# Kernel tuning notes

Hardware: AMD Instinct MI355X
Metric: run time of the kernel (lower is better)

Reference implementation:

```python
import jax, jax.numpy as jnp
import numpy as np

D = 1024
H = 16
HD = D // H
FF = 4096
B = 4
S = 1024
EPS = 1e-5


def layer_norm(x, g, b):
    mu = jnp.mean(x, axis=-1, keepdims=True)
    var = jnp.mean(jnp.square(x - mu), axis=-1, keepdims=True)
    return (x - mu) * jax.lax.rsqrt(var + EPS) * g + b


def setup_inputs() -> dict:
    key = jax.random.key(0)
    ks = jax.random.split(key, 16)
    s = 0.02
    return {
        "src": jax.random.normal(ks[0], (B, S, D), jnp.float32),
        "attn_bias": jax.random.normal(ks[1], (H, S, S), jnp.float32),
        "Wqkv": jax.random.normal(ks[2], (3 * D, D), jnp.float32) * s,
        "bqkv": jnp.zeros((3 * D,), jnp.float32),
        "Wo": jax.random.normal(ks[3], (D, D), jnp.float32) * s,
        "bo": jnp.zeros((D,), jnp.float32),
        "g1": jnp.ones((D,), jnp.float32),
        "b1n": jnp.zeros((D,), jnp.float32),
        "g2": jnp.ones((D,), jnp.float32),
        "b2n": jnp.zeros((D,), jnp.float32),
        "W1": jax.random.normal(ks[4], (FF, D), jnp.float32) * s,
        "b1": jnp.zeros((FF,), jnp.float32),
        "W2": jax.random.normal(ks[5], (D, FF), jnp.float32) * s,
        "b2": jnp.zeros((D,), jnp.float32),
    }


def reference(src, attn_bias, Wqkv, bqkv, Wo, bo, g1, b1n, g2, b2n, W1, b1, W2, b2):
    bsz, seq, _ = src.shape
    qkv = src @ Wqkv.T + bqkv                      # [B,S,3D]
    q, k, v = jnp.split(qkv, 3, axis=-1)
    q = q.reshape(bsz, seq, H, HD)
    k = k.reshape(bsz, seq, H, HD)
    v = v.reshape(bsz, seq, H, HD)
    scores = jnp.einsum('bthd,bshd->bhts', q, k) / np.sqrt(HD).astype(np.float32)
    scores = scores + attn_bias[None]              # 3D bias broadcast over batch
    w = jax.nn.softmax(scores, axis=-1)
    ctx = jnp.einsum('bhts,bshd->bthd', w, v).reshape(bsz, seq, D)
    attn_out = ctx @ Wo.T + bo
    x = layer_norm(src + attn_out, g1, b1n)
    ff = (jax.nn.gelu(x @ W1.T + b1, approximate=False)) @ W2.T + b2
    return layer_norm(x + ff, g2, b2n)
```

## Files before the change

### kernel.cpp

```cpp
#include <hip/hip_runtime.h>
#include <cstdint>

typedef unsigned short u16;
typedef __bf16 bf16x8 __attribute__((ext_vector_type(8)));
typedef float f32x4 __attribute__((ext_vector_type(4)));
typedef unsigned short u16x8 __attribute__((ext_vector_type(8)));
typedef unsigned short u16x4 __attribute__((ext_vector_type(4)));

__device__ __forceinline__ u16 f2b(float f) {
  union { float f; unsigned u; } x; x.f = f;
  unsigned r = (x.u + 0x7FFFu + ((x.u >> 16) & 1u)) >> 16;
  return (u16)r;
}
__device__ __forceinline__ float b2f(u16 v) {
  union { unsigned u; float f; } x; x.u = (unsigned)v << 16; return x.f;
}

__device__ __forceinline__ void gload_lds16(const void* g, void* l) {
  __builtin_amdgcn_global_load_lds(
      (__attribute__((address_space(1))) void*)(uintptr_t)g,
      (__attribute__((address_space(3))) void*)(uintptr_t)l, 16, 0, 0);
}

struct CastArgs {
  const float* in[5];
  u16* out[5];
  int cum[6];
};
__global__ void cast_multi(CastArgs a) {
  const int i = blockIdx.x * 256 + threadIdx.x;
  int r = 0;
#pragma unroll
  for (int k = 1; k < 5; ++k) r += (i >= a.cum[k]);
  const int local = i - a.cum[r];
  const float4 v0 = *(const float4*)(a.in[r] + (size_t)local * 8);
  const float4 v1 = *(const float4*)(a.in[r] + (size_t)local * 8 + 4);
  u16x8 o = {f2b(v0.x), f2b(v0.y), f2b(v0.z), f2b(v0.w),
             f2b(v1.x), f2b(v1.y), f2b(v1.z), f2b(v1.w)};
  *(u16x8*)(a.out[r] + (size_t)local * 8) = o;
}

template<bool GELU_ACT, bool WRITE_VT>
__global__ void gemm_nt(const u16* __restrict__ A, const u16* __restrict__ Bw,
                        const float* __restrict__ bias, u16* __restrict__ Cb,
                        u16* __restrict__ Vt, int M, int N, int K) {
  __shared__ u16 As[2][128 * 32];
  __shared__ u16 Bs[2][128 * 32];
  const int tid = threadIdx.x;
  const int lane = tid & 63, wid = tid >> 6;
  const int bm = blockIdx.y * 128, bn = blockIdx.x * 128;
  const int wm = wid >> 1, wn = wid & 1;
  const int r = lane & 15, g = lane >> 4;
  const int s4 = (r >> 1) & 3;

  auto stage = [&](int buf, int k0) {
#pragma unroll
    for (int i = 0; i < 2; ++i) {
      const int c = tid + i * 256;
      const int row = c >> 2, ch = c & 3;
      const int gs = ch ^ ((row >> 1) & 3);
      gload_lds16(A + (size_t)(bm + row) * K + k0 + gs * 8, &As[buf][c * 8]);
      gload_lds16(Bw + (size_t)(bn + row) * K + k0 + gs * 8, &Bs[buf][c * 8]);
    }
  };

  f32x4 acc[4][4] = {};
  stage(0, 0);
  __syncthreads();
  const int nk = K >> 5;
  int cur = 0;
  for (int kt = 0; kt < nk; ++kt) {
    if (kt + 1 < nk) stage(cur ^ 1, (kt + 1) * 32);
    bf16x8 af[4], bfr[4];
#pragma unroll
    for (int m = 0; m < 4; ++m)
      af[m] = *(const bf16x8*)&As[cur][(wm * 64 + m * 16 + r) * 32 + (g ^ s4) * 8];
#pragma unroll
    for (int n = 0; n < 4; ++n)
      bfr[n] = *(const bf16x8*)&Bs[cur][(wn * 64 + n * 16 + r) * 32 + (g ^ s4) * 8];
#pragma unroll
    for (int m = 0; m < 4; ++m)
#pragma unroll
      for (int n = 0; n < 4; ++n)
        acc[m][n] = __builtin_amdgcn_mfma_f32_16x16x32_bf16(af[m], bfr[n], acc[m][n], 0, 0, 0);
    __syncthreads();
    cur ^= 1;
  }
#pragma unroll
  for (int m = 0; m < 4; ++m) {
    const int row0 = bm + wm * 64 + m * 16 + g * 4;
#pragma unroll
    for (int n = 0; n < 4; ++n) {
      const int col = bn + wn * 64 + n * 16 + r;
      const float bv = bias[col];
      if (WRITE_VT && col >= 2048) {
        const int hv = col - 2048;
        const int bb = row0 >> 10, s0 = row0 & 1023;
        u16x4 ov;
#pragma unroll
        for (int j = 0; j < 4; ++j) ov[j] = f2b(acc[m][n][j] + bv);
        *(u16x4*)(Vt + (((size_t)(bb * 16 + (hv >> 6))) * 64 + (hv & 63)) * 1024 + s0) = ov;
      } else {
#pragma unroll
        for (int j = 0; j < 4; ++j) {
          float v = acc[m][n][j] + bv;
          if (GELU_ACT) v = 0.5f * v * (1.f + erff(v * 0.70710678118654752f));
          Cb[(size_t)(row0 + j) * N + col] = f2b(v);
        }
      }
    }
  }
}

__global__ void gemm_nt_splitk(const u16* __restrict__ A, const u16* __restrict__ Bw,
                               u16* __restrict__ parts, int M, int N, int K, int Kc) {
  __shared__ u16 As[2][128 * 32];
  __shared__ u16 Bs[2][128 * 32];
  const int tid = threadIdx.x;
  const int lane = tid & 63, wid = tid >> 6;
  const int bm = blockIdx.y * 128, bn = blockIdx.x * 128;
  const int kbase = blockIdx.z * Kc;
  const int wm = wid >> 1, wn = wid & 1;
  const int r = lane & 15, g = lane >> 4;
  const int s4 = (r >> 1) & 3;

  auto stage = [&](int buf, int k0) {
#pragma unroll
    for (int i = 0; i < 2; ++i) {
      const int c = tid + i * 256;
      const int row = c >> 2, ch = c & 3;
      const int gs = ch ^ ((row >> 1) & 3);
      gload_lds16(A + (size_t)(bm + row) * K + k0 + gs * 8, &As[buf][c * 8]);
      gload_lds16(Bw + (size_t)(bn + row) * K + k0 + gs * 8, &Bs[buf][c * 8]);
    }
  };

  f32x4 acc[4][4] = {};
  stage(0, kbase);
  __syncthreads();
  const int nk = Kc >> 5;
  int cur = 0;
  for (int kt = 0; kt < nk; ++kt) {
    if (kt + 1 < nk) stage(cur ^ 1, kbase + (kt + 1) * 32);
    bf16x8 af[4], bfr[4];
#pragma unroll
    for (int m = 0; m < 4; ++m)
      af[m] = *(const bf16x8*)&As[cur][(wm * 64 + m * 16 + r) * 32 + (g ^ s4) * 8];
#pragma unroll
    for (int n = 0; n < 4; ++n)
      bfr[n] = *(const bf16x8*)&Bs[cur][(wn * 64 + n * 16 + r) * 32 + (g ^ s4) * 8];
#pragma unroll
    for (int m = 0; m < 4; ++m)
#pragma unroll
      for (int n = 0; n < 4; ++n)
        acc[m][n] = __builtin_amdgcn_mfma_f32_16x16x32_bf16(af[m], bfr[n], acc[m][n], 0, 0, 0);
    __syncthreads();
    cur ^= 1;
  }
  u16* Cp = parts + (size_t)blockIdx.z * M * N;
#pragma unroll
  for (int m = 0; m < 4; ++m) {
    const int row0 = bm + wm * 64 + m * 16 + g * 4;
#pragma unroll
    for (int n = 0; n < 4; ++n) {
      const int col = bn + wn * 64 + n * 16 + r;
#pragma unroll
      for (int j = 0; j < 4; ++j)
        Cp[(size_t)(row0 + j) * N + col] = f2b(acc[m][n][j]);
    }
  }
}

__global__ __launch_bounds__(256) void attn_kernel(
    const u16* __restrict__ qkv, const u16* __restrict__ Vt,
    const float* __restrict__ bias, u16* __restrict__ ctx) {
  const int fid = blockIdx.x;
  const int xcd = fid & 7, slot = fid >> 3;
  const int G = xcd * 64 + (slot >> 2);
  const int b = slot & 3;
  const int h = G >> 5;
  const int q0 = (G & 31) * 32;
  const int tid = threadIdx.x;
  const int lane = tid & 63, wid = tid >> 6;
  const int r = lane & 15, g = lane >> 4;
  const int bh = b * 16 + h;

  __shared__ __align__(16) u16 PB[2][16 * 1024];

  const size_t qb0 = (size_t)(b * 1024 + q0 + r) * 3072 + h * 64;
  const size_t qb1 = (size_t)(b * 1024 + q0 + 16 + r) * 3072 + h * 64;
  const bf16x8 aq00 = *(const bf16x8*)(qkv + qb0 + g * 8);
  const bf16x8 aq01 = *(const bf16x8*)(qkv + qb0 + 32 + g * 8);
  const bf16x8 aq10 = *(const bf16x8*)(qkv + qb1 + g * 8);
  const bf16x8 aq11 = *(const bf16x8*)(qkv + qb1 + 32 + g * 8);

  const int n0 = wid * 256;

  const u16* kptr = qkv + (size_t)(b * 1024 + n0 + r) * 3072 + 1024 + h * 64;
  const size_t kstep = (size_t)16 * 3072;
  bf16x8 k0a = *(const bf16x8*)(kptr + g * 8);
  bf16x8 k1a = *(const bf16x8*)(kptr + 32 + g * 8);
#pragma unroll
  for (int nt = 0; nt < 16; ++nt) {
    bf16x8 k0b, k1b;
    if (nt + 1 < 16) {
      const u16* kn = kptr + (size_t)(nt + 1) * kstep;
      k0b = *(const bf16x8*)(kn + g * 8);
      k1b = *(const bf16x8*)(kn + 32 + g * 8);
    }
    f32x4 a0 = {0.f, 0.f, 0.f, 0.f}, a1 = {0.f, 0.f, 0.f, 0.f};
    a0 = __builtin_amdgcn_mfma_f32_16x16x32_bf16(k0a, aq00, a0, 0, 0, 0);
    a1 = __builtin_amdgcn_mfma_f32_16x16x32_bf16(k0a, aq10, a1, 0, 0, 0);
    a0 = __builtin_amdgcn_mfma_f32_16x16x32_bf16(k1a, aq01, a0, 0, 0, 0);
    a1 = __builtin_amdgcn_mfma_f32_16x16x32_bf16(k1a, aq11, a1, 0, 0, 0);
    const int col = n0 + nt * 16 + g * 4;
    const int idx = r * 1024 + (col ^ ((r & 15) << 3));
    u16x4 o0 = {f2b(a0[0] * 0.125f), f2b(a0[1] * 0.125f),
                f2b(a0[2] * 0.125f), f2b(a0[3] * 0.125f)};
    u16x4 o1 = {f2b(a1[0] * 0.125f), f2b(a1[1] * 0.125f),
                f2b(a1[2] * 0.125f), f2b(a1[3] * 0.125f)};
    *(u16x4*)&PB[0][idx] = o0;
    *(u16x4*)&PB[1][idx] = o1;
    k0a = k0b;
    k1a = k1b;
  }
  __syncthreads();

#pragma unroll
  for (int tr = 0; tr < 8; ++tr) {
    const int t = tr & 1, rr = tr >> 1;
    const int row = wid * 4 + rr;
    const int swz = (row & 15) << 3;
    u16* prow = &PB[t][row * 1024];
    const float* brow = bias + ((size_t)h * 1024 + q0 + t * 16 + row) * 1024;
    const int c0 = lane * 16;
    float bb[16];
    *(float4*)&bb[0]  = *(const float4*)(brow + c0);
    *(float4*)&bb[4]  = *(const float4*)(brow + c0 + 4);
    *(float4*)&bb[8]  = *(const float4*)(brow + c0 + 8);
    *(float4*)&bb[12] = *(const float4*)(brow + c0 + 12);
    const u16x8 v0 = *(const u16x8*)&prow[c0 ^ swz];
    const u16x8 v1 = *(const u16x8*)&prow[(c0 + 8) ^ swz];
    float f[16];
#pragma unroll
    for (int k = 0; k < 8; ++k) {
      f[k]     = b2f(v0[k]) + bb[k];
      f[8 + k] = b2f(v1[k]) + bb[8 + k];
    }
    float m = f[0];
#pragma unroll
    for (int k = 1; k < 16; ++k) m = fmaxf(m, f[k]);
    m = fmaxf(m, __shfl_xor(m, 1));  m = fmaxf(m, __shfl_xor(m, 2));
    m = fmaxf(m, __shfl_xor(m, 4));  m = fmaxf(m, __shfl_xor(m, 8));
    m = fmaxf(m, __shfl_xor(m, 16)); m = fmaxf(m, __shfl_xor(m, 32));
    float s = 0.f;
#pragma unroll
    for (int k = 0; k < 16; ++k) { f[k] = __expf(f[k] - m); s += f[k]; }
    s += __shfl_xor(s, 1);  s += __shfl_xor(s, 2);
    s += __shfl_xor(s, 4);  s += __shfl_xor(s, 8);
    s += __shfl_xor(s, 16); s += __shfl_xor(s, 32);
    const float inv = 1.f / s;
    u16x8 o0, o1;
#pragma unroll
    for (int k = 0; k < 8; ++k) {
      o0[k] = f2b(f[k] * inv);
      o1[k] = f2b(f[8 + k] * inv);
    }
    *(u16x8*)&prow[c0 ^ swz] = o0;
    *(u16x8*)&prow[(c0 + 8) ^ swz] = o1;
  }
  __syncthreads();

  f32x4 oa = {0.f, 0.f, 0.f, 0.f}, ob = {0.f, 0.f, 0.f, 0.f};
  const u16* vrow = Vt + ((size_t)bh * 64 + wid * 16 + r) * 1024;
  bf16x8 vba = *(const bf16x8*)(vrow + g * 8);
#pragma unroll
  for (int ks = 0; ks < 32; ++ks) {
    bf16x8 vbb;
    if (ks + 1 < 32) vbb = *(const bf16x8*)(vrow + (ks + 1) * 32 + g * 8);
    const int off = (ks * 32 + g * 8) ^ ((r & 15) << 3);
    const bf16x8 pa0 = *(const bf16x8*)&PB[0][r * 1024 + off];
    const bf16x8 pa1 = *(const bf16x8*)&PB[1][r * 1024 + off];
    oa = __builtin_amdgcn_mfma_f32_16x16x32_bf16(pa0, vba, oa, 0, 0, 0);
    ob = __builtin_amdgcn_mfma_f32_16x16x32_bf16(pa1, vba, ob, 0, 0, 0);
    vba = vbb;
  }
#pragma unroll
  for (int j = 0; j < 4; ++j) {
    ctx[(size_t)(b * 1024 + q0 + g * 4 + j) * 1024 + h * 64 + wid * 16 + r] = f2b(oa[j]);
    ctx[(size_t)(b * 1024 + q0 + 16 + g * 4 + j) * 1024 + h * 64 + wid * 16 + r] = f2b(ob[j]);
  }
}

template<int NP, bool RESID_BF16>
__global__ void ln_sum_kernel(const u16* __restrict__ parts,
                              const void* __restrict__ resid,
                              const float* __restrict__ cbias,
                              const float* __restrict__ gw, const float* __restrict__ bw,
                              float* __restrict__ outf, u16* __restrict__ outb) {
  const int row = blockIdx.x, tid = threadIdx.x;
  const size_t off = (size_t)row * 1024 + tid * 4;
  float4 v;
  if (RESID_BF16) {
    const u16x4 rb = *(const u16x4*)((const u16*)resid + off);
    v.x = b2f(rb[0]); v.y = b2f(rb[1]); v.z = b2f(rb[2]); v.w = b2f(rb[3]);
  } else {
    v = *(const float4*)((const float*)resid + off);
  }
  const float4 cb = *(const float4*)(cbias + tid * 4);
  v.x += cb.x; v.y += cb.y; v.z += cb.z; v.w += cb.w;
#pragma unroll
  for (int p = 0; p < NP; ++p) {
    const u16x4 a = *(const u16x4*)(parts + (size_t)p * 4096 * 1024 + off);
    v.x += b2f(a[0]); v.y += b2f(a[1]); v.z += b2f(a[2]); v.w += b2f(a[3]);
  }
  float s = v.x + v.y + v.z + v.w;
  float q = v.x * v.x + v.y * v.y + v.z * v.z + v.w * v.w;
#pragma unroll
  for (int m = 32; m >= 1; m >>= 1) { s += __shfl_xor(s, m); q += __shfl_xor(q, m); }
  __shared__ float rs[4], rq[4];
  if ((tid & 63) == 0) { rs[tid >> 6] = s; rq[tid >> 6] = q; }
  __syncthreads();
  s = rs[0] + rs[1] + rs[2] + rs[3];
  q = rq[0] + rq[1] + rq[2] + rq[3];
  const float mu = s * (1.f / 1024.f);
  const float inv = rsqrtf(q * (1.f / 1024.f) - mu * mu + 1e-5f);
  const float4 g4 = *(const float4*)(gw + tid * 4);
  const float4 b4 = *(const float4*)(bw + tid * 4);
  float4 o;
  o.x = (v.x - mu) * inv * g4.x + b4.x;
  o.y = (v.y - mu) * inv * g4.y + b4.y;
  o.z = (v.z - mu) * inv * g4.z + b4.z;
  o.w = (v.w - mu) * inv * g4.w + b4.w;
  if (outf) *(float4*)(outf + off) = o;
  if (outb) {
    u16x4 ob = {f2b(o.x), f2b(o.y), f2b(o.z), f2b(o.w)};
    *(u16x4*)(outb + off) = ob;
  }
}

extern "C" void kernel_launch(void* const* d_in, const int* in_sizes, int n_in,
                              void* d_out, int out_size, void* d_ws, size_t ws_size,
                              hipStream_t stream) {
  (void)in_sizes; (void)n_in; (void)out_size; (void)ws_size;
  const float* src   = (const float*)d_in[0];
  const float* abias = (const float*)d_in[1];
  const float* Wqkv  = (const float*)d_in[2];
  const float* bqkv  = (const float*)d_in[3];
  const float* Wo    = (const float*)d_in[4];
  const float* bo    = (const float*)d_in[5];
  const float* g1    = (const float*)d_in[6];
  const float* b1n   = (const float*)d_in[7];
  const float* g2    = (const float*)d_in[8];
  const float* b2n   = (const float*)d_in[9];
  const float* W1    = (const float*)d_in[10];
  const float* b1    = (const float*)d_in[11];
  const float* W2    = (const float*)d_in[12];
  const float* b2    = (const float*)d_in[13];
  float* out = (float*)d_out;

  char* ws = (char*)d_ws;
  const size_t MB = 1024 * 1024;
  u16* srcb  = (u16*)(ws + 0 * MB);
  u16* ctxb  = (u16*)(ws + 0 * MB);
  u16* xb    = (u16*)(ws + 0 * MB);
  u16* Wqkvb = (u16*)(ws + 8 * MB);
  u16* Wob   = (u16*)(ws + 14 * MB);
  u16* W2b   = (u16*)(ws + 24 * MB);
  u16* qkvb  = (u16*)(ws + 32 * MB);
  u16* Vt    = (u16*)(ws + 56 * MB);
  u16* hb    = (u16*)(ws + 32 * MB);
  u16* parts = (u16*)(ws + 64 * MB);
  u16* W1b   = (u16*)(ws + 96 * MB);

  CastArgs ca;
  ca.in[0] = src;  ca.out[0] = srcb;
  ca.in[1] = Wqkv; ca.out[1] = Wqkvb;
  ca.in[2] = Wo;   ca.out[2] = Wob;
  ca.in[3] = W1;   ca.out[3] = W1b;
  ca.in[4] = W2;   ca.out[4] = W2b;
  ca.cum[0] = 0;
  ca.cum[1] = 524288;
  ca.cum[2] = 524288 + 393216;
  ca.cum[3] = 524288 + 393216 + 131072;
  ca.cum[4] = 524288 + 393216 + 131072 + 524288;
  ca.cum[5] = 2097152;
  cast_multi<<<2097152 / 256, 256, 0, stream>>>(ca);

  gemm_nt<false, true><<<dim3(3072 / 128, 4096 / 128), 256, 0, stream>>>(
      srcb, Wqkvb, bqkv, qkvb, Vt, 4096, 3072, 1024);
  attn_kernel<<<2048, 256, 0, stream>>>(qkvb, Vt, abias, ctxb);
  gemm_nt_splitk<<<dim3(1024 / 128, 4096 / 128, 2), 256, 0, stream>>>(
      ctxb, Wob, parts, 4096, 1024, 1024, 512);
  ln_sum_kernel<2, false><<<4096, 256, 0, stream>>>(
      parts, src, bo, g1, b1n, nullptr, xb);
  gemm_nt<true, false><<<dim3(4096 / 128, 4096 / 128), 256, 0, stream>>>(
      xb, W1b, b1, hb, nullptr, 4096, 4096, 1024);
  gemm_nt_splitk<<<dim3(1024 / 128, 4096 / 128, 2), 256, 0, stream>>>(
      hb, W2b, parts, 4096, 1024, 4096, 2048);
  ln_sum_kernel<2, true><<<4096, 256, 0, stream>>>(
      parts, xb, b2, g2, b2n, out, nullptr);
}
```

Baseline: 271.9 us.

## Process 64 query rows per attention block instead of 32

The attention kernel's query tile grows from 32 to 64 rows per block, so each loaded K and V fragment feeds four MFMAs instead of two and the grid is halved. The score buffer in shared memory doubles to 128 KB, and each wave now runs softmax over its own 16-row tile. This cuts K/V global reads per query, but lowers occupancy to at most one block per CU because of LDS use, and leaves fewer blocks to spread across CUs.

After: 323.9 us. 1.19x slower.

```diff
diff --git a/kernel.cpp b/kernel.cpp
--- a/kernel.cpp
+++ b/kernel.cpp
@@ -176,23 +176,24 @@
     const float* __restrict__ bias, u16* __restrict__ ctx) {
   const int fid = blockIdx.x;
   const int xcd = fid & 7, slot = fid >> 3;
-  const int G = xcd * 64 + (slot >> 2);
+  const int G = xcd * 32 + (slot >> 2);
   const int b = slot & 3;
-  const int h = G >> 5;
-  const int q0 = (G & 31) * 32;
+  const int h = G >> 4;
+  const int q0 = (G & 15) * 64;
   const int tid = threadIdx.x;
   const int lane = tid & 63, wid = tid >> 6;
   const int r = lane & 15, g = lane >> 4;
   const int bh = b * 16 + h;
 
-  __shared__ __align__(16) u16 PB[2][16 * 1024];
-
-  const size_t qb0 = (size_t)(b * 1024 + q0 + r) * 3072 + h * 64;
-  const size_t qb1 = (size_t)(b * 1024 + q0 + 16 + r) * 3072 + h * 64;
-  const bf16x8 aq00 = *(const bf16x8*)(qkv + qb0 + g * 8);
-  const bf16x8 aq01 = *(const bf16x8*)(qkv + qb0 + 32 + g * 8);
-  const bf16x8 aq10 = *(const bf16x8*)(qkv + qb1 + g * 8);
-  const bf16x8 aq11 = *(const bf16x8*)(qkv + qb1 + 32 + g * 8);
+  __shared__ __align__(16) u16 PB[4][16 * 1024];
+
+  bf16x8 aq0[4], aq1[4];
+#pragma unroll
+  for (int t = 0; t < 4; ++t) {
+    const size_t qb = (size_t)(b * 1024 + q0 + t * 16 + r) * 3072 + h * 64;
+    aq0[t] = *(const bf16x8*)(qkv + qb + g * 8);
+    aq1[t] = *(const bf16x8*)(qkv + qb + 32 + g * 8);
+  }
 
   const int n0 = wid * 256;
 
@@ -208,31 +209,31 @@
       k0b = *(const bf16x8*)(kn + g * 8);
       k1b = *(const bf16x8*)(kn + 32 + g * 8);
     }
-    f32x4 a0 = {0.f, 0.f, 0.f, 0.f}, a1 = {0.f, 0.f, 0.f, 0.f};
-    a0 = __builtin_amdgcn_mfma_f32_16x16x32_bf16(k0a, aq00, a0, 0, 0, 0);
-    a1 = __builtin_amdgcn_mfma_f32_16x16x32_bf16(k0a, aq10, a1, 0, 0, 0);
-    a0 = __builtin_amdgcn_mfma_f32_16x16x32_bf16(k1a, aq01, a0, 0, 0, 0);
-    a1 = __builtin_amdgcn_mfma_f32_16x16x32_bf16(k1a, aq11, a1, 0, 0, 0);
+    f32x4 a[4];
+#pragma unroll
+    for (int t = 0; t < 4; ++t) {
+      a[t] = f32x4{0.f, 0.f, 0.f, 0.f};
+      a[t] = __builtin_amdgcn_mfma_f32_16x16x32_bf16(k0a, aq0[t], a[t], 0, 0, 0);
+      a[t] = __builtin_amdgcn_mfma_f32_16x16x32_bf16(k1a, aq1[t], a[t], 0, 0, 0);
+    }
     const int col = n0 + nt * 16 + g * 4;
     const int idx = r * 1024 + (col ^ ((r & 15) << 3));
-    u16x4 o0 = {f2b(a0[0] * 0.125f), f2b(a0[1] * 0.125f),
-                f2b(a0[2] * 0.125f), f2b(a0[3] * 0.125f)};
-    u16x4 o1 = {f2b(a1[0] * 0.125f), f2b(a1[1] * 0.125f),
-                f2b(a1[2] * 0.125f), f2b(a1[3] * 0.125f)};
-    *(u16x4*)&PB[0][idx] = o0;
-    *(u16x4*)&PB[1][idx] = o1;
+#pragma unroll
+    for (int t = 0; t < 4; ++t) {
+      u16x4 o = {f2b(a[t][0] * 0.125f), f2b(a[t][1] * 0.125f),
+                 f2b(a[t][2] * 0.125f), f2b(a[t][3] * 0.125f)};
+      *(u16x4*)&PB[t][idx] = o;
+    }
     k0a = k0b;
     k1a = k1b;
   }
   __syncthreads();
 
 #pragma unroll
-  for (int tr = 0; tr < 8; ++tr) {
-    const int t = tr & 1, rr = tr >> 1;
-    const int row = wid * 4 + rr;
-    const int swz = (row & 15) << 3;
-    u16* prow = &PB[t][row * 1024];
-    const float* brow = bias + ((size_t)h * 1024 + q0 + t * 16 + row) * 1024;
+  for (int lr = 0; lr < 16; ++lr) {
+    const int swz = lr << 3;
+    u16* prow = &PB[wid][lr * 1024];
+    const float* brow = bias + ((size_t)h * 1024 + q0 + wid * 16 + lr) * 1024;
     const int c0 = lane * 16;
     float bb[16];
     *(float4*)&bb[0]  = *(const float4*)(brow + c0);
@@ -271,7 +272,7 @@
   }
   __syncthreads();
 
-  f32x4 oa = {0.f, 0.f, 0.f, 0.f}, ob = {0.f, 0.f, 0.f, 0.f};
+  f32x4 oacc[4] = {};
   const u16* vrow = Vt + ((size_t)bh * 64 + wid * 16 + r) * 1024;
   bf16x8 vba = *(const bf16x8*)(vrow + g * 8);
 #pragma unroll
@@ -279,17 +280,19 @@
     bf16x8 vbb;
     if (ks + 1 < 32) vbb = *(const bf16x8*)(vrow + (ks + 1) * 32 + g * 8);
     const int off = (ks * 32 + g * 8) ^ ((r & 15) << 3);
-    const bf16x8 pa0 = *(const bf16x8*)&PB[0][r * 1024 + off];
-    const bf16x8 pa1 = *(const bf16x8*)&PB[1][r * 1024 + off];
-    oa = __builtin_amdgcn_mfma_f32_16x16x32_bf16(pa0, vba, oa, 0, 0, 0);
-    ob = __builtin_amdgcn_mfma_f32_16x16x32_bf16(pa1, vba, ob, 0, 0, 0);
+#pragma unroll
+    for (int t = 0; t < 4; ++t) {
+      const bf16x8 pa = *(const bf16x8*)&PB[t][r * 1024 + off];
+      oacc[t] = __builtin_amdgcn_mfma_f32_16x16x32_bf16(pa, vba, oacc[t], 0, 0, 0);
+    }
     vba = vbb;
   }
 #pragma unroll
-  for (int j = 0; j < 4; ++j) {
-    ctx[(size_t)(b * 1024 + q0 + g * 4 + j) * 1024 + h * 64 + wid * 16 + r] = f2b(oa[j]);
-    ctx[(size_t)(b * 1024 + q0 + 16 + g * 4 + j) * 1024 + h * 64 + wid * 16 + r] = f2b(ob[j]);
-  }
+  for (int t = 0; t < 4; ++t)
+#pragma unroll
+    for (int j = 0; j < 4; ++j)
+      ctx[(size_t)(b * 1024 + q0 + t * 16 + g * 4 + j) * 1024 + h * 64 + wid * 16 + r] =
+          f2b(oacc[t][j]);
 }
 
 template<int NP, bool RESID_BF16>
@@ -389,7 +392,7 @@
 
   gemm_nt<false, true><<<dim3(3072 / 128, 4096 / 128), 256, 0, stream>>>(
       srcb, Wqkvb, bqkv, qkvb, Vt, 4096, 3072, 1024);
-  attn_kernel<<<2048, 256, 0, stream>>>(qkvb, Vt, abias, ctxb);
+  attn_kernel<<<1024, 256, 0, stream>>>(qkvb, Vt, abias, ctxb);
   gemm_nt_splitk<<<dim3(1024 / 128, 4096 / 128, 2), 256, 0, stream>>>(
       ctxb, Wob, parts, 4096, 1024, 1024, 512);
   ln_sum_kernel<2, false><<<4096, 256, 0, stream>>>(
```

## Restructure attention kernel into single-wave blocks over 16 queries without barriers

Applied to the files above, without the earlier changes.

The attention kernel now launches 4096 one-wave blocks, each handling 16 query rows over the full key range, instead of 2048 four-wave blocks handling 32 rows. Because one wave owns its whole LDS score tile, the __syncthreads barriers are replaced by LDS waitcnt fences, and each wave computes all four 16-column slices of the PV product. The aim is to remove block-level synchronisation and halve LDS per block. The cost is that every block re-reads all of K and V for only 16 queries, roughly doubling that global traffic. The score loop's one-ahead K prefetch also reads one tile past the end of the key range on its last iteration.

Result: slower. 349.5 us (+28.5%).

```diff
diff --git a/kernel.cpp b/kernel.cpp
--- a/kernel.cpp
+++ b/kernel.cpp
@@ -171,69 +171,53 @@
   }
 }
 
-__global__ __launch_bounds__(256) void attn_kernel(
+__global__ __launch_bounds__(64) void attn_kernel(
     const u16* __restrict__ qkv, const u16* __restrict__ Vt,
     const float* __restrict__ bias, u16* __restrict__ ctx) {
   const int fid = blockIdx.x;
   const int xcd = fid & 7, slot = fid >> 3;
-  const int G = xcd * 64 + (slot >> 2);
+  const int G = xcd * 128 + (slot >> 2);
   const int b = slot & 3;
-  const int h = G >> 5;
-  const int q0 = (G & 31) * 32;
-  const int tid = threadIdx.x;
-  const int lane = tid & 63, wid = tid >> 6;
+  const int h = G >> 6;
+  const int q0 = (G & 63) * 16;
+  const int lane = threadIdx.x;
   const int r = lane & 15, g = lane >> 4;
   const int bh = b * 16 + h;
 
-  __shared__ __align__(16) u16 PB[2][16 * 1024];
-
-  const size_t qb0 = (size_t)(b * 1024 + q0 + r) * 3072 + h * 64;
-  const size_t qb1 = (size_t)(b * 1024 + q0 + 16 + r) * 3072 + h * 64;
-  const bf16x8 aq00 = *(const bf16x8*)(qkv + qb0 + g * 8);
-  const bf16x8 aq01 = *(const bf16x8*)(qkv + qb0 + 32 + g * 8);
-  const bf16x8 aq10 = *(const bf16x8*)(qkv + qb1 + g * 8);
-  const bf16x8 aq11 = *(const bf16x8*)(qkv + qb1 + 32 + g * 8);
-
-  const int n0 = wid * 256;
-
-  const u16* kptr = qkv + (size_t)(b * 1024 + n0 + r) * 3072 + 1024 + h * 64;
+  __shared__ __align__(16) u16 PB[16 * 1024];
+
+  const size_t qb = (size_t)(b * 1024 + q0 + r) * 3072 + h * 64;
+  const bf16x8 aq0 = *(const bf16x8*)(qkv + qb + g * 8);
+  const bf16x8 aq1 = *(const bf16x8*)(qkv + qb + 32 + g * 8);
+
+  const u16* kptr = qkv + (size_t)(b * 1024 + r) * 3072 + 1024 + h * 64;
   const size_t kstep = (size_t)16 * 3072;
   bf16x8 k0a = *(const bf16x8*)(kptr + g * 8);
   bf16x8 k1a = *(const bf16x8*)(kptr + 32 + g * 8);
-#pragma unroll
-  for (int nt = 0; nt < 16; ++nt) {
-    bf16x8 k0b, k1b;
-    if (nt + 1 < 16) {
-      const u16* kn = kptr + (size_t)(nt + 1) * kstep;
-      k0b = *(const bf16x8*)(kn + g * 8);
-      k1b = *(const bf16x8*)(kn + 32 + g * 8);
-    }
-    f32x4 a0 = {0.f, 0.f, 0.f, 0.f}, a1 = {0.f, 0.f, 0.f, 0.f};
-    a0 = __builtin_amdgcn_mfma_f32_16x16x32_bf16(k0a, aq00, a0, 0, 0, 0);
-    a1 = __builtin_amdgcn_mfma_f32_16x16x32_bf16(k0a, aq10, a1, 0, 0, 0);
-    a0 = __builtin_amdgcn_mfma_f32_16x16x32_bf16(k1a, aq01, a0, 0, 0, 0);
-    a1 = __builtin_amdgcn_mfma_f32_16x16x32_bf16(k1a, aq11, a1, 0, 0, 0);
-    const int col = n0 + nt * 16 + g * 4;
-    const int idx = r * 1024 + (col ^ ((r & 15) << 3));
-    u16x4 o0 = {f2b(a0[0] * 0.125f), f2b(a0[1] * 0.125f),
-                f2b(a0[2] * 0.125f), f2b(a0[3] * 0.125f)};
-    u16x4 o1 = {f2b(a1[0] * 0.125f), f2b(a1[1] * 0.125f),
-                f2b(a1[2] * 0.125f), f2b(a1[3] * 0.125f)};
-    *(u16x4*)&PB[0][idx] = o0;
-    *(u16x4*)&PB[1][idx] = o1;
+#pragma unroll 8
+  for (int nt = 0; nt < 64; ++nt) {
+    const u16* kn = kptr + (size_t)(nt + 1) * kstep;
+    const bf16x8 k0b = *(const bf16x8*)(kn + g * 8);
+    const bf16x8 k1b = *(const bf16x8*)(kn + 32 + g * 8);
+    f32x4 a = {0.f, 0.f, 0.f, 0.f};
+    a = __builtin_amdgcn_mfma_f32_16x16x32_bf16(k0a, aq0, a, 0, 0, 0);
+    a = __builtin_amdgcn_mfma_f32_16x16x32_bf16(k1a, aq1, a, 0, 0, 0);
+    const int col = nt * 16 + g * 4;
+    const int idx = r * 1024 + (col ^ (r << 3));
+    u16x4 o = {f2b(a[0] * 0.125f), f2b(a[1] * 0.125f),
+               f2b(a[2] * 0.125f), f2b(a[3] * 0.125f)};
+    *(u16x4*)&PB[idx] = o;
     k0a = k0b;
     k1a = k1b;
   }
-  __syncthreads();
-
-#pragma unroll
-  for (int tr = 0; tr < 8; ++tr) {
-    const int t = tr & 1, rr = tr >> 1;
-    const int row = wid * 4 + rr;
-    const int swz = (row & 15) << 3;
-    u16* prow = &PB[t][row * 1024];
-    const float* brow = bias + ((size_t)h * 1024 + q0 + t * 16 + row) * 1024;
-    const int c0 = lane * 16;
+  asm volatile("s_waitcnt lgkmcnt(0)" ::: "memory");
+
+  const int c0 = lane * 16;
+#pragma unroll 4
+  for (int lr = 0; lr < 16; ++lr) {
+    const int swz = lr << 3;
+    u16* prow = &PB[lr * 1024];
+    const float* brow = bias + ((size_t)h * 1024 + q0 + lr) * 1024;
     float bb[16];
     *(float4*)&bb[0]  = *(const float4*)(brow + c0);
     *(float4*)&bb[4]  = *(const float4*)(brow + c0 + 4);
@@ -269,26 +253,31 @@
     *(u16x8*)&prow[c0 ^ swz] = o0;
     *(u16x8*)&prow[(c0 + 8) ^ swz] = o1;
   }
-  __syncthreads();
-
-  f32x4 oa = {0.f, 0.f, 0.f, 0.f}, ob = {0.f, 0.f, 0.f, 0.f};
-  const u16* vrow = Vt + ((size_t)bh * 64 + wid * 16 + r) * 1024;
-  bf16x8 vba = *(const bf16x8*)(vrow + g * 8);
-#pragma unroll
+  asm volatile("s_waitcnt lgkmcnt(0)" ::: "memory");
+
+  f32x4 o0 = {0.f, 0.f, 0.f, 0.f}, o1 = {0.f, 0.f, 0.f, 0.f};
+  f32x4 o2 = {0.f, 0.f, 0.f, 0.f}, o3 = {0.f, 0.f, 0.f, 0.f};
+  const u16* vbase = Vt + ((size_t)bh * 64 + r) * 1024;
+#pragma unroll 4
   for (int ks = 0; ks < 32; ++ks) {
-    bf16x8 vbb;
-    if (ks + 1 < 32) vbb = *(const bf16x8*)(vrow + (ks + 1) * 32 + g * 8);
-    const int off = (ks * 32 + g * 8) ^ ((r & 15) << 3);
-    const bf16x8 pa0 = *(const bf16x8*)&PB[0][r * 1024 + off];
-    const bf16x8 pa1 = *(const bf16x8*)&PB[1][r * 1024 + off];
-    oa = __builtin_amdgcn_mfma_f32_16x16x32_bf16(pa0, vba, oa, 0, 0, 0);
-    ob = __builtin_amdgcn_mfma_f32_16x16x32_bf16(pa1, vba, ob, 0, 0, 0);
-    vba = vbb;
+    const int off = (ks * 32 + g * 8) ^ (r << 3);
+    const bf16x8 pa = *(const bf16x8*)&PB[r * 1024 + off];
+    const bf16x8 vb0 = *(const bf16x8*)(vbase + 0 * 16384 + ks * 32 + g * 8);
+    const bf16x8 vb1 = *(const bf16x8*)(vbase + 1 * 16384 + ks * 32 + g * 8);
+    const bf16x8 vb2 = *(const bf16x8*)(vbase + 2 * 16384 + ks * 32 + g * 8);
+    const bf16x8 vb3 = *(const bf16x8*)(vbase + 3 * 16384 + ks * 32 + g * 8);
+    o0 = __builtin_amdgcn_mfma_f32_16x16x32_bf16(pa, vb0, o0, 0, 0, 0);
+    o1 = __builtin_amdgcn_mfma_f32_16x16x32_bf16(pa, vb1, o1, 0, 0, 0);
+    o2 = __builtin_amdgcn_mfma_f32_16x16x32_bf16(pa, vb2, o2, 0, 0, 0);
+    o3 = __builtin_amdgcn_mfma_f32_16x16x32_bf16(pa, vb3, o3, 0, 0, 0);
   }
 #pragma unroll
   for (int j = 0; j < 4; ++j) {
-    ctx[(size_t)(b * 1024 + q0 + g * 4 + j) * 1024 + h * 64 + wid * 16 + r] = f2b(oa[j]);
-    ctx[(size_t)(b * 1024 + q0 + 16 + g * 4 + j) * 1024 + h * 64 + wid * 16 + r] = f2b(ob[j]);
+    const size_t orow = (size_t)(b * 1024 + q0 + g * 4 + j) * 1024 + h * 64 + r;
+    ctx[orow]      = f2b(o0[j]);
+    ctx[orow + 16] = f2b(o1[j]);
+    ctx[orow + 32] = f2b(o2[j]);
+    ctx[orow + 48] = f2b(o3[j]);
   }
 }
 
@@ -389,7 +378,7 @@
 
   gemm_nt<false, true><<<dim3(3072 / 128, 4096 / 128), 256, 0, stream>>>(
       srcb, Wqkvb, bqkv, qkvb, Vt, 4096, 3072, 1024);
-  attn_kernel<<<2048, 256, 0, stream>>>(qkvb, Vt, abias, ctxb);
+  attn_kernel<<<4096, 64, 0, stream>>>(qkvb, Vt, abias, ctxb);
   gemm_nt_splitk<<<dim3(1024 / 128, 4096 / 128, 2), 256, 0, stream>>>(
       ctxb, Wob, parts, 4096, 1024, 1024, 512);
   ln_sum_kernel<2, false><<<4096, 256, 0, stream>>>(
```

## Split attention over two KV halves with a separate log-sum-exp merge kernel

Applied to the files above, without the earlier changes.

Each attention block now covers half of the key range, which doubles the grid and halves LDS use per block (32KB instead of 64KB), so more blocks can be resident per CU. Each block writes unnormalized partial outputs plus per-row max and sum, and a new merge kernel rescales and combines the two halves into ctx. In exchange it adds an extra kernel launch and a round trip of partials through global memory, and the partials are rounded to bf16 before the merge.

After: 277.6 us. 2.1% more time.

```diff
diff --git a/kernel.cpp b/kernel.cpp
--- a/kernel.cpp
+++ b/kernel.cpp
@@ -173,19 +173,24 @@
 
 __global__ __launch_bounds__(256) void attn_kernel(
     const u16* __restrict__ qkv, const u16* __restrict__ Vt,
-    const float* __restrict__ bias, u16* __restrict__ ctx) {
+    const float* __restrict__ bias, u16* __restrict__ po,
+    float* __restrict__ pm, float* __restrict__ pl) {
   const int fid = blockIdx.x;
   const int xcd = fid & 7, slot = fid >> 3;
-  const int G = xcd * 64 + (slot >> 2);
+  const int G = xcd * 128 + (slot >> 2);
   const int b = slot & 3;
-  const int h = G >> 5;
-  const int q0 = (G & 31) * 32;
+  const int h = G >> 6;
+  const int qt = (G >> 1) & 31;
+  const int sp = G & 1;
+  const int q0 = qt * 32;
+  const int kv0 = sp * 512;
   const int tid = threadIdx.x;
   const int lane = tid & 63, wid = tid >> 6;
   const int r = lane & 15, g = lane >> 4;
   const int bh = b * 16 + h;
-
-  __shared__ __align__(16) u16 PB[2][16 * 1024];
+  const int pidx = (b * 16 + h) * 32 + qt;
+
+  __shared__ __align__(16) u16 PB[2][16 * 512];
 
   const size_t qb0 = (size_t)(b * 1024 + q0 + r) * 3072 + h * 64;
   const size_t qb1 = (size_t)(b * 1024 + q0 + 16 + r) * 3072 + h * 64;
@@ -194,16 +199,16 @@
   const bf16x8 aq10 = *(const bf16x8*)(qkv + qb1 + g * 8);
   const bf16x8 aq11 = *(const bf16x8*)(qkv + qb1 + 32 + g * 8);
 
-  const int n0 = wid * 256;
-
-  const u16* kptr = qkv + (size_t)(b * 1024 + n0 + r) * 3072 + 1024 + h * 64;
+  const int n0 = wid * 128;
+
+  const u16* kptr = qkv + (size_t)(b * 1024 + kv0 + n0 + r) * 3072 + 1024 + h * 64;
   const size_t kstep = (size_t)16 * 3072;
   bf16x8 k0a = *(const bf16x8*)(kptr + g * 8);
   bf16x8 k1a = *(const bf16x8*)(kptr + 32 + g * 8);
 #pragma unroll
-  for (int nt = 0; nt < 16; ++nt) {
+  for (int nt = 0; nt < 8; ++nt) {
     bf16x8 k0b, k1b;
-    if (nt + 1 < 16) {
+    if (nt + 1 < 8) {
       const u16* kn = kptr + (size_t)(nt + 1) * kstep;
       k0b = *(const bf16x8*)(kn + g * 8);
       k1b = *(const bf16x8*)(kn + 32 + g * 8);
@@ -214,7 +219,7 @@
     a0 = __builtin_amdgcn_mfma_f32_16x16x32_bf16(k1a, aq01, a0, 0, 0, 0);
     a1 = __builtin_amdgcn_mfma_f32_16x16x32_bf16(k1a, aq11, a1, 0, 0, 0);
     const int col = n0 + nt * 16 + g * 4;
-    const int idx = r * 1024 + (col ^ ((r & 15) << 3));
+    const int idx = r * 512 + (col ^ ((r & 15) << 3));
     u16x4 o0 = {f2b(a0[0] * 0.125f), f2b(a0[1] * 0.125f),
                 f2b(a0[2] * 0.125f), f2b(a0[3] * 0.125f)};
     u16x4 o1 = {f2b(a1[0] * 0.125f), f2b(a1[1] * 0.125f),
@@ -231,65 +236,82 @@
     const int t = tr & 1, rr = tr >> 1;
     const int row = wid * 4 + rr;
     const int swz = (row & 15) << 3;
-    u16* prow = &PB[t][row * 1024];
-    const float* brow = bias + ((size_t)h * 1024 + q0 + t * 16 + row) * 1024;
-    const int c0 = lane * 16;
-    float bb[16];
-    *(float4*)&bb[0]  = *(const float4*)(brow + c0);
-    *(float4*)&bb[4]  = *(const float4*)(brow + c0 + 4);
-    *(float4*)&bb[8]  = *(const float4*)(brow + c0 + 8);
-    *(float4*)&bb[12] = *(const float4*)(brow + c0 + 12);
+    u16* prow = &PB[t][row * 512];
+    const float* brow = bias + ((size_t)h * 1024 + q0 + t * 16 + row) * 1024 + kv0;
+    const int c0 = lane * 8;
+    float bb[8];
+    *(float4*)&bb[0] = *(const float4*)(brow + c0);
+    *(float4*)&bb[4] = *(const float4*)(brow + c0 + 4);
     const u16x8 v0 = *(const u16x8*)&prow[c0 ^ swz];
-    const u16x8 v1 = *(const u16x8*)&prow[(c0 + 8) ^ swz];
-    float f[16];
-#pragma unroll
-    for (int k = 0; k < 8; ++k) {
-      f[k]     = b2f(v0[k]) + bb[k];
-      f[8 + k] = b2f(v1[k]) + bb[8 + k];
-    }
+    float f[8];
+#pragma unroll
+    for (int k = 0; k < 8; ++k) f[k] = b2f(v0[k]) + bb[k];
     float m = f[0];
 #pragma unroll
-    for (int k = 1; k < 16; ++k) m = fmaxf(m, f[k]);
+    for (int k = 1; k < 8; ++k) m = fmaxf(m, f[k]);
     m = fmaxf(m, __shfl_xor(m, 1));  m = fmaxf(m, __shfl_xor(m, 2));
     m = fmaxf(m, __shfl_xor(m, 4));  m = fmaxf(m, __shfl_xor(m, 8));
     m = fmaxf(m, __shfl_xor(m, 16)); m = fmaxf(m, __shfl_xor(m, 32));
     float s = 0.f;
 #pragma unroll
-    for (int k = 0; k < 16; ++k) { f[k] = __expf(f[k] - m); s += f[k]; }
+    for (int k = 0; k < 8; ++k) { f[k] = __expf(f[k] - m); s += f[k]; }
     s += __shfl_xor(s, 1);  s += __shfl_xor(s, 2);
     s += __shfl_xor(s, 4);  s += __shfl_xor(s, 8);
     s += __shfl_xor(s, 16); s += __shfl_xor(s, 32);
-    const float inv = 1.f / s;
-    u16x8 o0, o1;
-#pragma unroll
-    for (int k = 0; k < 8; ++k) {
-      o0[k] = f2b(f[k] * inv);
-      o1[k] = f2b(f[8 + k] * inv);
-    }
+    u16x8 o0;
+#pragma unroll
+    for (int k = 0; k < 8; ++k) o0[k] = f2b(f[k]);
     *(u16x8*)&prow[c0 ^ swz] = o0;
-    *(u16x8*)&prow[(c0 + 8) ^ swz] = o1;
+    if (lane == 0) {
+      const size_t mi = (size_t)(sp * 2048 + pidx) * 32 + t * 16 + row;
+      pm[mi] = m;
+      pl[mi] = s;
+    }
   }
   __syncthreads();
 
   f32x4 oa = {0.f, 0.f, 0.f, 0.f}, ob = {0.f, 0.f, 0.f, 0.f};
-  const u16* vrow = Vt + ((size_t)bh * 64 + wid * 16 + r) * 1024;
+  const u16* vrow = Vt + ((size_t)bh * 64 + wid * 16 + r) * 1024 + kv0;
   bf16x8 vba = *(const bf16x8*)(vrow + g * 8);
 #pragma unroll
-  for (int ks = 0; ks < 32; ++ks) {
+  for (int ks = 0; ks < 16; ++ks) {
     bf16x8 vbb;
-    if (ks + 1 < 32) vbb = *(const bf16x8*)(vrow + (ks + 1) * 32 + g * 8);
+    if (ks + 1 < 16) vbb = *(const bf16x8*)(vrow + (ks + 1) * 32 + g * 8);
     const int off = (ks * 32 + g * 8) ^ ((r & 15) << 3);
-    const bf16x8 pa0 = *(const bf16x8*)&PB[0][r * 1024 + off];
-    const bf16x8 pa1 = *(const bf16x8*)&PB[1][r * 1024 + off];
+    const bf16x8 pa0 = *(const bf16x8*)&PB[0][r * 512 + off];
+    const bf16x8 pa1 = *(const bf16x8*)&PB[1][r * 512 + off];
     oa = __builtin_amdgcn_mfma_f32_16x16x32_bf16(pa0, vba, oa, 0, 0, 0);
     ob = __builtin_amdgcn_mfma_f32_16x16x32_bf16(pa1, vba, ob, 0, 0, 0);
     vba = vbb;
   }
+  u16* pot = po + (size_t)(sp * 2048 + pidx) * 32 * 64;
 #pragma unroll
   for (int j = 0; j < 4; ++j) {
-    ctx[(size_t)(b * 1024 + q0 + g * 4 + j) * 1024 + h * 64 + wid * 16 + r] = f2b(oa[j]);
-    ctx[(size_t)(b * 1024 + q0 + 16 + g * 4 + j) * 1024 + h * 64 + wid * 16 + r] = f2b(ob[j]);
-  }
+    pot[(g * 4 + j) * 64 + wid * 16 + r]      = f2b(oa[j]);
+    pot[(16 + g * 4 + j) * 64 + wid * 16 + r] = f2b(ob[j]);
+  }
+}
+
+__global__ void attn_merge(const u16* __restrict__ po, const float* __restrict__ pm,
+                           const float* __restrict__ pl, u16* __restrict__ ctx) {
+  const int pidx = blockIdx.x;
+  const int t = threadIdx.x;
+  const int rl = t >> 3, d0 = (t & 7) * 8;
+  const size_t i1 = (size_t)pidx * 32 + rl;
+  const size_t i2 = (size_t)(2048 + pidx) * 32 + rl;
+  const float m1 = pm[i1], m2 = pm[i2];
+  const float l1 = pl[i1], l2 = pl[i2];
+  const float M = fmaxf(m1, m2);
+  const float w1 = __expf(m1 - M), w2 = __expf(m2 - M);
+  const float inv = 1.f / (w1 * l1 + w2 * l2);
+  const u16x8 a = *(const u16x8*)(po + i1 * 64 + d0);
+  const u16x8 c = *(const u16x8*)(po + i2 * 64 + d0);
+  u16x8 o;
+#pragma unroll
+  for (int k = 0; k < 8; ++k)
+    o[k] = f2b((w1 * b2f(a[k]) + w2 * b2f(c[k])) * inv);
+  const int b = pidx >> 9, h = (pidx >> 5) & 15, qt = pidx & 31;
+  *(u16x8*)(ctx + (size_t)(b * 1024 + qt * 32 + rl) * 1024 + h * 64 + d0) = o;
 }
 
 template<int NP, bool RESID_BF16>
@@ -371,6 +393,9 @@
   u16* Vt    = (u16*)(ws + 56 * MB);
   u16* hb    = (u16*)(ws + 32 * MB);
   u16* parts = (u16*)(ws + 64 * MB);
+  u16* po    = (u16*)(ws + 64 * MB);
+  float* pm  = (float*)(ws + 80 * MB);
+  float* pl  = (float*)(ws + 81 * MB);
   u16* W1b   = (u16*)(ws + 96 * MB);
 
   CastArgs ca;
@@ -389,7 +414,8 @@
 
   gemm_nt<false, true><<<dim3(3072 / 128, 4096 / 128), 256, 0, stream>>>(
       srcb, Wqkvb, bqkv, qkvb, Vt, 4096, 3072, 1024);
-  attn_kernel<<<2048, 256, 0, stream>>>(qkvb, Vt, abias, ctxb);
+  attn_kernel<<<4096, 256, 0, stream>>>(qkvb, Vt, abias, po, pm, pl);
+  attn_merge<<<2048, 256, 0, stream>>>(po, pm, pl, ctxb);
   gemm_nt_splitk<<<dim3(1024 / 128, 4096 / 128, 2), 256, 0, stream>>>(
       ctxb, Wob, parts, 4096, 1024, 1024, 512);
   ln_sum_kernel<2, false><<<4096, 256, 0, stream>>>(
```
